# Performance work log

Measured on AMD Instinct MI355X. Metric: run time of the kernel, lower is better.

The kernel has to match this reference:

```python
import jax, jax.numpy as jnp
import numpy as np


def _greedy_match(d):
    # d: [S, S] pairwise distances. Greedy bipartite match: repeatedly take
    # global argmin, record pred_row -> gt_col, mask out that row and column.
    S = d.shape[0]

    def body(i, carry):
        dm, matches = carry
        m = jnp.argmin(dm.reshape(-1))
        r = m // S
        c = m % S
        matches = matches.at[r].set(c)
        dm = dm.at[r, :].set(jnp.inf)
        dm = dm.at[:, c].set(jnp.inf)
        return dm, matches

    _, matches = jax.lax.fori_loop(0, S, body, (d, jnp.zeros((S,), jnp.int32)))
    return matches


def setup_inputs() -> dict:
    key = jax.random.key(0)
    k1, k2 = jax.random.split(key)
    bs, seq_len, n_sources, input_dim = 8, 4096, 4, 257
    predictions = jax.random.normal(k1, (bs, seq_len, n_sources, input_dim), jnp.float32)
    ground_truths = jax.random.normal(k2, (bs, seq_len, n_sources, input_dim), jnp.float32)
    return {"predictions": predictions, "ground_truths": ground_truths}


def reference(predictions, ground_truths):
    # predictions, ground_truths: [bs, seq_len, S, D]
    bs, seq_len, S, D = predictions.shape
    # Flatten each source's full time-frequency signal: [bs, S, seq_len*D]
    p = jnp.transpose(predictions, (0, 2, 1, 3)).reshape(bs, S, seq_len * D)
    g = jnp.transpose(ground_truths, (0, 2, 1, 3)).reshape(bs, S, seq_len * D)

    # Euclidean cdist between pred sources and gt sources: [bs, S, S]
    d2 = (jnp.sum(p * p, axis=-1)[:, :, None]
          + jnp.sum(g * g, axis=-1)[:, None, :]
          - 2.0 * jnp.einsum('bsk,btk->bst', p, g))
    dists = jnp.sqrt(jnp.maximum(d2, 0.0))

    # Greedy assignment (ranks are monotone in distance, so matching on the
    # distances directly is identical to matching on the argsort-rank matrix).
    matches = jax.vmap(_greedy_match)(jax.lax.stop_gradient(dists))  # [bs, S] int32

    # Per-(batch, pred-source) distance to its matched gt source:
    # torch.norm(pred[b] - gt_match[b]) == euclidean dist of flattened vectors.
    gm = jnp.take_along_axis(g, matches[:, :, None], axis=1)  # [bs, S, seq_len*D]
    per = jnp.linalg.norm(p - gm, axis=-1)  # [bs, S]

    return jnp.sum(per) / bs
```

## Files before the change

### kernel.cpp

```cpp
#include <hip/hip_runtime.h>
#include <math.h>

#define BS 8
#define T  4096
#define D  257
#define SD 1028
#define K  (T * D)
#define NACC 24
#define BPB 256
#define NBLK (BS * BPB)
#define CHUNK 4112
#define NACC 24

__global__ __launch_bounds__(256) void zero_ws_kernel(float* ws) {
    int i = blockIdx.x * blockDim.x + threadIdx.x;
    if (i < BS * NACC) ws[i] = 0.0f;
}

__device__ __forceinline__ void process_pos(const float* __restrict__ Pb,
                                            const float* __restrict__ Gb,
                                            int i, float* acc) {
    const int t = i / D;
    const int d = i - t * D;
    const float* p = Pb + (size_t)t * SD + d;
    const float* g = Gb + (size_t)t * SD + d;
    const float p0 = __builtin_nontemporal_load(p);
    const float p1 = __builtin_nontemporal_load(p + D);
    const float p2 = __builtin_nontemporal_load(p + 2 * D);
    const float p3 = __builtin_nontemporal_load(p + 3 * D);
    const float g0 = __builtin_nontemporal_load(g);
    const float g1 = __builtin_nontemporal_load(g + D);
    const float g2 = __builtin_nontemporal_load(g + 2 * D);
    const float g3 = __builtin_nontemporal_load(g + 3 * D);
    acc[0] = fmaf(p0, p0, acc[0]);  acc[1] = fmaf(p1, p1, acc[1]);
    acc[2] = fmaf(p2, p2, acc[2]);  acc[3] = fmaf(p3, p3, acc[3]);
    acc[4] = fmaf(g0, g0, acc[4]);  acc[5] = fmaf(g1, g1, acc[5]);
    acc[6] = fmaf(g2, g2, acc[6]);  acc[7] = fmaf(g3, g3, acc[7]);
    acc[ 8] = fmaf(p0, g0, acc[ 8]); acc[ 9] = fmaf(p0, g1, acc[ 9]);
    acc[10] = fmaf(p0, g2, acc[10]); acc[11] = fmaf(p0, g3, acc[11]);
    acc[12] = fmaf(p1, g0, acc[12]); acc[13] = fmaf(p1, g1, acc[13]);
    acc[14] = fmaf(p1, g2, acc[14]); acc[15] = fmaf(p1, g3, acc[15]);
    acc[16] = fmaf(p2, g0, acc[16]); acc[17] = fmaf(p2, g1, acc[17]);
    acc[18] = fmaf(p2, g2, acc[18]); acc[19] = fmaf(p2, g3, acc[19]);
    acc[20] = fmaf(p3, g0, acc[20]); acc[21] = fmaf(p3, g1, acc[21]);
    acc[22] = fmaf(p3, g2, acc[22]); acc[23] = fmaf(p3, g3, acc[23]);
}

template <int DIRECT>
__global__ __launch_bounds__(256) void partial_kernel(const float* __restrict__ P,
                                                      const float* __restrict__ G,
                                                      float* __restrict__ ws) {
    const int tid  = threadIdx.x;
    const int lane = tid & 63;
    const int wv   = tid >> 6;
    const int b    = blockIdx.x >> 8;
    const int c    = blockIdx.x & (BPB - 1);

    const float* __restrict__ Pb = P + (size_t)b * T * SD;
    const float* __restrict__ Gb = G + (size_t)b * T * SD;

    float acc[NACC];
    #pragma unroll
    for (int k = 0; k < NACC; ++k) acc[k] = 0.0f;

    const int base = c * CHUNK;
    #pragma unroll 2
    for (int it = 0; it < CHUNK / 256; ++it)
        process_pos(Pb, Gb, base + it * 256 + tid, acc);

    __shared__ float sm[4][NACC];
    #pragma unroll
    for (int k = 0; k < NACC; ++k) {
        float v = acc[k];
        #pragma unroll
        for (int o = 32; o > 0; o >>= 1) v += __shfl_down(v, o, 64);
        if (lane == 0) sm[wv][k] = v;
    }
    __syncthreads();
    if (tid < NACC) {
        float v = sm[0][tid] + sm[1][tid] + sm[2][tid] + sm[3][tid];
        if (DIRECT) ws[blockIdx.x * NACC + tid] = v;
        else        atomicAdd(&ws[b * NACC + tid], v);
    }
}

__device__ __forceinline__ float greedy_total(const float* w8x24 ) {
    float total = 0.f;
    for (int b = 0; b < BS; ++b) {
        const float* w = w8x24 + b * NACC;
        float dist[16];
        for (int s = 0; s < 4; ++s)
            for (int t = 0; t < 4; ++t) {
                float d2 = w[s] + w[4 + t] - 2.f * w[8 + s * 4 + t];
                dist[s * 4 + t] = sqrtf(fmaxf(d2, 0.f));
            }
        bool rdone[4] = {false, false, false, false};
        bool cdone[4] = {false, false, false, false};
        for (int it = 0; it < 4; ++it) {
            float best = INFINITY; int br = 0, bc = 0;
            bool found = false;
            for (int s = 0; s < 4; ++s) {
                if (rdone[s]) continue;
                for (int t = 0; t < 4; ++t) {
                    if (cdone[t]) continue;
                    float v = dist[s * 4 + t];
                    if (!found || v < best) { best = v; br = s; bc = t; found = true; }
                }
            }
            total += best;
            rdone[br] = true; cdone[bc] = true;
        }
    }
    return total * 0.125f;
}

__global__ __launch_bounds__(256) void finalize_direct_kernel(const float* __restrict__ ws,
                                                              float* __restrict__ out) {
    __shared__ float wsm[BS * NACC];
    const int t = threadIdx.x;
    if (t < BS * NACC) {
        const int b = t / NACC, k = t - b * NACC;
        float v = 0.f;
        for (int j = 0; j < BPB; ++j)
            v += ws[(size_t)((b << 8) | j) * NACC + k];
        wsm[t] = v;
    }
    __syncthreads();
    if (t == 0) *out = greedy_total(wsm);
}

__global__ void finalize_atomic_kernel(const float* __restrict__ ws, float* __restrict__ out) {
    if (threadIdx.x != 0 || blockIdx.x != 0) return;
    *out = greedy_total(ws);
}

extern "C" void kernel_launch(void* const* d_in, const int* in_sizes, int n_in,
                              void* d_out, int out_size, void* d_ws, size_t ws_size,
                              hipStream_t stream) {
    const float* P = (const float*)d_in[0];
    const float* G = (const float*)d_in[1];
    float* out = (float*)d_out;
    float* ws  = (float*)d_ws;

    if (ws_size >= (size_t)NBLK * NACC * sizeof(float)) {
        partial_kernel<1><<<NBLK, 256, 0, stream>>>(P, G, ws);
        finalize_direct_kernel<<<1, 256, 0, stream>>>(ws, out);
    } else {
        zero_ws_kernel<<<1, 256, 0, stream>>>(ws);
        partial_kernel<0><<<NBLK, 256, 0, stream>>>(P, G, ws);
        finalize_atomic_kernel<<<1, 64, 0, stream>>>(ws, out);
    }
}
```

Measured before the change: 82.66 us.

## Restructure partial reduction into row-wise vector loads with software double-buffering

New measurement: 75.34 us. -8.9%, faster.

```diff
diff --git a/kernel.cpp b/kernel.cpp
--- a/kernel.cpp
+++ b/kernel.cpp
@@ -5,45 +5,62 @@
 #define T  4096
 #define D  257
 #define SD 1028
-#define K  (T * D)
 #define NACC 24
-#define BPB 256
-#define NBLK (BS * BPB)
-#define CHUNK 4112
-#define NACC 24
+#define RPB 32
+#define CPB 128
+#define NBLK (BS * CPB)
+
+typedef float v4f __attribute__((ext_vector_type(4)));
 
 __global__ __launch_bounds__(256) void zero_ws_kernel(float* ws) {
     int i = blockIdx.x * blockDim.x + threadIdx.x;
     if (i < BS * NACC) ws[i] = 0.0f;
 }
 
-__device__ __forceinline__ void process_pos(const float* __restrict__ Pb,
-                                            const float* __restrict__ Gb,
-                                            int i, float* acc) {
-    const int t = i / D;
-    const int d = i - t * D;
-    const float* p = Pb + (size_t)t * SD + d;
-    const float* g = Gb + (size_t)t * SD + d;
-    const float p0 = __builtin_nontemporal_load(p);
-    const float p1 = __builtin_nontemporal_load(p + D);
-    const float p2 = __builtin_nontemporal_load(p + 2 * D);
-    const float p3 = __builtin_nontemporal_load(p + 3 * D);
-    const float g0 = __builtin_nontemporal_load(g);
-    const float g1 = __builtin_nontemporal_load(g + D);
-    const float g2 = __builtin_nontemporal_load(g + 2 * D);
-    const float g3 = __builtin_nontemporal_load(g + 3 * D);
-    acc[0] = fmaf(p0, p0, acc[0]);  acc[1] = fmaf(p1, p1, acc[1]);
-    acc[2] = fmaf(p2, p2, acc[2]);  acc[3] = fmaf(p3, p3, acc[3]);
-    acc[4] = fmaf(g0, g0, acc[4]);  acc[5] = fmaf(g1, g1, acc[5]);
-    acc[6] = fmaf(g2, g2, acc[6]);  acc[7] = fmaf(g3, g3, acc[7]);
-    acc[ 8] = fmaf(p0, g0, acc[ 8]); acc[ 9] = fmaf(p0, g1, acc[ 9]);
-    acc[10] = fmaf(p0, g2, acc[10]); acc[11] = fmaf(p0, g3, acc[11]);
-    acc[12] = fmaf(p1, g0, acc[12]); acc[13] = fmaf(p1, g1, acc[13]);
-    acc[14] = fmaf(p1, g2, acc[14]); acc[15] = fmaf(p1, g3, acc[15]);
-    acc[16] = fmaf(p2, g0, acc[16]); acc[17] = fmaf(p2, g1, acc[17]);
-    acc[18] = fmaf(p2, g2, acc[18]); acc[19] = fmaf(p2, g3, acc[19]);
-    acc[20] = fmaf(p3, g0, acc[20]); acc[21] = fmaf(p3, g1, acc[21]);
-    acc[22] = fmaf(p3, g2, acc[22]); acc[23] = fmaf(p3, g3, acc[23]);
+__device__ __forceinline__ void issue8(const float* pp, const float* gg,
+                                       v4f& p0, v4f& p1, v4f& p2, v4f& p3,
+                                       v4f& g0, v4f& g1, v4f& g2, v4f& g3) {
+    asm volatile(
+        "global_load_dwordx4 %0, %8, off\n\t"
+        "global_load_dwordx4 %1, %8, off offset:1028\n\t"
+        "global_load_dwordx4 %2, %8, off offset:2056\n\t"
+        "global_load_dwordx4 %3, %8, off offset:3084\n\t"
+        "global_load_dwordx4 %4, %9, off\n\t"
+        "global_load_dwordx4 %5, %9, off offset:1028\n\t"
+        "global_load_dwordx4 %6, %9, off offset:2056\n\t"
+        "global_load_dwordx4 %7, %9, off offset:3084"
+        : "=&v"(p0), "=&v"(p1), "=&v"(p2), "=&v"(p3),
+          "=&v"(g0), "=&v"(g1), "=&v"(g2), "=&v"(g3)
+        : "v"(pp), "v"(gg));
+}
+
+#define WAIT8 do { asm volatile("s_waitcnt vmcnt(8)" ::: "memory"); \
+                   __builtin_amdgcn_sched_barrier(0); } while (0)
+#define WAIT0 do { asm volatile("s_waitcnt vmcnt(0)" ::: "memory"); \
+                   __builtin_amdgcn_sched_barrier(0); } while (0)
+
+__device__ __forceinline__ void consume8(const v4f& p0, const v4f& p1,
+                                         const v4f& p2, const v4f& p3,
+                                         const v4f& g0, const v4f& g1,
+                                         const v4f& g2, const v4f& g3,
+                                         float* acc) {
+    #pragma unroll
+    for (int e = 0; e < 4; ++e) {
+        const float a0 = p0[e], a1 = p1[e], a2 = p2[e], a3 = p3[e];
+        const float b0 = g0[e], b1 = g1[e], b2 = g2[e], b3 = g3[e];
+        acc[0] = fmaf(a0, a0, acc[0]);  acc[1] = fmaf(a1, a1, acc[1]);
+        acc[2] = fmaf(a2, a2, acc[2]);  acc[3] = fmaf(a3, a3, acc[3]);
+        acc[4] = fmaf(b0, b0, acc[4]);  acc[5] = fmaf(b1, b1, acc[5]);
+        acc[6] = fmaf(b2, b2, acc[6]);  acc[7] = fmaf(b3, b3, acc[7]);
+        acc[ 8] = fmaf(a0, b0, acc[ 8]); acc[ 9] = fmaf(a0, b1, acc[ 9]);
+        acc[10] = fmaf(a0, b2, acc[10]); acc[11] = fmaf(a0, b3, acc[11]);
+        acc[12] = fmaf(a1, b0, acc[12]); acc[13] = fmaf(a1, b1, acc[13]);
+        acc[14] = fmaf(a1, b2, acc[14]); acc[15] = fmaf(a1, b3, acc[15]);
+        acc[16] = fmaf(a2, b0, acc[16]); acc[17] = fmaf(a2, b1, acc[17]);
+        acc[18] = fmaf(a2, b2, acc[18]); acc[19] = fmaf(a2, b3, acc[19]);
+        acc[20] = fmaf(a3, b0, acc[20]); acc[21] = fmaf(a3, b1, acc[21]);
+        acc[22] = fmaf(a3, b2, acc[22]); acc[23] = fmaf(a3, b3, acc[23]);
+    }
 }
 
 template <int DIRECT>
@@ -53,8 +70,8 @@
     const int tid  = threadIdx.x;
     const int lane = tid & 63;
     const int wv   = tid >> 6;
-    const int b    = blockIdx.x >> 8;
-    const int c    = blockIdx.x & (BPB - 1);
+    const int b    = blockIdx.x >> 7;
+    const int c    = blockIdx.x & (CPB - 1);
 
     const float* __restrict__ Pb = P + (size_t)b * T * SD;
     const float* __restrict__ Gb = G + (size_t)b * T * SD;
@@ -63,10 +80,45 @@
     #pragma unroll
     for (int k = 0; k < NACC; ++k) acc[k] = 0.0f;
 
-    const int base = c * CHUNK;
-    #pragma unroll 2
-    for (int it = 0; it < CHUNK / 256; ++it)
-        process_pos(Pb, Gb, base + it * 256 + tid, acc);
+    const int rowbase = c * RPB + wv * 8;
+    const float* pa = Pb + (size_t)rowbase * SD + (lane << 2);
+    const float* ga = Gb + (size_t)rowbase * SD + (lane << 2);
+
+    v4f A0, A1, A2, A3, A4, A5, A6, A7;
+    v4f B0, B1, B2, B3, B4, B5, B6, B7;
+
+    issue8(pa,      ga,      A0, A1, A2, A3, A4, A5, A6, A7);
+    issue8(pa + SD, ga + SD, B0, B1, B2, B3, B4, B5, B6, B7);
+    #pragma unroll
+    for (int k = 0; k < 3; ++k) {
+        WAIT8; consume8(A0, A1, A2, A3, A4, A5, A6, A7, acc);
+        issue8(pa + (size_t)(2 + 2 * k) * SD, ga + (size_t)(2 + 2 * k) * SD,
+               A0, A1, A2, A3, A4, A5, A6, A7);
+        WAIT8; consume8(B0, B1, B2, B3, B4, B5, B6, B7, acc);
+        issue8(pa + (size_t)(3 + 2 * k) * SD, ga + (size_t)(3 + 2 * k) * SD,
+               B0, B1, B2, B3, B4, B5, B6, B7);
+    }
+    WAIT8; consume8(A0, A1, A2, A3, A4, A5, A6, A7, acc);
+    WAIT0; consume8(B0, B1, B2, B3, B4, B5, B6, B7, acc);
+
+    if (tid < RPB) {
+        const float* p = Pb + (size_t)(c * RPB + tid) * SD + 256;
+        const float* g = Gb + (size_t)(c * RPB + tid) * SD + 256;
+        const float a0 = p[0], a1 = p[D], a2 = p[2 * D], a3 = p[3 * D];
+        const float b0 = g[0], b1 = g[D], b2 = g[2 * D], b3 = g[3 * D];
+        acc[0] = fmaf(a0, a0, acc[0]);  acc[1] = fmaf(a1, a1, acc[1]);
+        acc[2] = fmaf(a2, a2, acc[2]);  acc[3] = fmaf(a3, a3, acc[3]);
+        acc[4] = fmaf(b0, b0, acc[4]);  acc[5] = fmaf(b1, b1, acc[5]);
+        acc[6] = fmaf(b2, b2, acc[6]);  acc[7] = fmaf(b3, b3, acc[7]);
+        acc[ 8] = fmaf(a0, b0, acc[ 8]); acc[ 9] = fmaf(a0, b1, acc[ 9]);
+        acc[10] = fmaf(a0, b2, acc[10]); acc[11] = fmaf(a0, b3, acc[11]);
+        acc[12] = fmaf(a1, b0, acc[12]); acc[13] = fmaf(a1, b1, acc[13]);
+        acc[14] = fmaf(a1, b2, acc[14]); acc[15] = fmaf(a1, b3, acc[15]);
+        acc[16] = fmaf(a2, b0, acc[16]); acc[17] = fmaf(a2, b1, acc[17]);
+        acc[18] = fmaf(a2, b2, acc[18]); acc[19] = fmaf(a2, b3, acc[19]);
+        acc[20] = fmaf(a3, b0, acc[20]); acc[21] = fmaf(a3, b1, acc[21]);
+        acc[22] = fmaf(a3, b2, acc[22]); acc[23] = fmaf(a3, b3, acc[23]);
+    }
 
     __shared__ float sm[4][NACC];
     #pragma unroll
@@ -121,8 +173,8 @@
     if (t < BS * NACC) {
         const int b = t / NACC, k = t - b * NACC;
         float v = 0.f;
-        for (int j = 0; j < BPB; ++j)
-            v += ws[(size_t)((b << 8) | j) * NACC + k];
+        for (int j = 0; j < CPB; ++j)
+            v += ws[(size_t)(b * CPB + j) * NACC + k];
         wsm[t] = v;
     }
     __syncthreads();
```
